# Kernel tuning notes

Measured on AMD Instinct MI355X. Metric: run time of the kernel, lower is better.

The kernel has to match this reference:

```python
import jax, jax.numpy as jnp
import numpy as np

N_NODES = 50000

def gcn_conv(x, edge_index, W, b):
    # PyG GCNConv default: add self-loops, symmetric norm D^-1/2 (A+I) D^-1/2, then XW + b
    n = x.shape[0]
    loop = jnp.arange(n, dtype=edge_index.dtype)
    src = jnp.concatenate([edge_index[0], loop])
    dst = jnp.concatenate([edge_index[1], loop])
    deg = jax.ops.segment_sum(jnp.ones_like(src, dtype=x.dtype), dst, num_segments=n)
    dinv = jnp.where(deg > 0, jax.lax.rsqrt(jnp.maximum(deg, 1e-12)), 0.0)
    norm = dinv[src] * dinv[dst]                      # [E+N]
    h = x @ W                                          # [N, d_out]
    msg = h[src] * norm[:, None]                       # gather + scale
    out = jax.ops.segment_sum(msg, dst, num_segments=n)  # scatter-add
    return out + b

def leaky(x):
    return jnp.where(x >= 0, x, 0.01 * x)

def setup_inputs() -> dict:
    key = jax.random.key(0)
    ks = jax.random.split(key, 10)
    x = jax.random.normal(ks[0], (N_NODES, 128), dtype=jnp.float32)
    edge_index = jax.random.randint(ks[1], (2, 800000), 0, N_NODES, dtype=jnp.int64)
    W1 = jax.random.normal(ks[2], (128, 512), dtype=jnp.float32) / np.sqrt(128)
    b1 = jnp.zeros((512,), dtype=jnp.float32)
    W3 = jax.random.normal(ks[3], (512, 128), dtype=jnp.float32) / np.sqrt(512)
    b3 = jnp.zeros((128,), dtype=jnp.float32)
    fc1_w = jax.random.normal(ks[4], (256, 128), dtype=jnp.float32) * np.sqrt(2.0 / 256)
    fc1_b = jnp.zeros((256,), dtype=jnp.float32)
    fc2_w = jax.random.normal(ks[5], (1, 256), dtype=jnp.float32) * np.sqrt(2.0 / 1)
    fc2_b = jnp.zeros((1,), dtype=jnp.float32)
    return {"x": x, "edge_index": edge_index, "W1": W1, "b1": b1, "W3": W3, "b3": b3,
            "fc1_w": fc1_w, "fc1_b": fc1_b, "fc2_w": fc2_w, "fc2_b": fc2_b}

def reference(x, edge_index, W1, b1, W3, b3, fc1_w, fc1_b, fc2_w, fc2_b):
    h = leaky(gcn_conv(x, edge_index, W1, b1))
    h = leaky(gcn_conv(h, edge_index, W3, b3))
    h = leaky(h @ fc1_w.T + fc1_b)
    h = h @ fc2_w.T + fc2_b
    return h.squeeze(-1)  # [N]
```

## Files before the change

### kernel.cpp

```cpp
#include <hip/hip_runtime.h>
#include <hip/hip_fp16.h>

typedef _Float16 f16x8 __attribute__((ext_vector_type(8)));
typedef __attribute__((ext_vector_type(4))) float f32x4;

static __device__ __forceinline__ float leaky(float v) { return v >= 0.f ? v : 0.01f * v; }

__global__ __launch_bounds__(256) void k_prep_all(
    const float* __restrict__ x, const float* __restrict__ W1, const float* __restrict__ W3,
    const float* __restrict__ fc1w, const float* __restrict__ fc2b,
    const int* __restrict__ dst, int* __restrict__ bucket_cnt,
    float* __restrict__ out, __half* __restrict__ x16, __half* __restrict__ t2,
    _Float16* __restrict__ W1f, _Float16* __restrict__ W3f, _Float16* __restrict__ F1f,
    int N, int E)
{
    __shared__ int bcnt[256];
    bcnt[threadIdx.x] = 0;
    __syncthreads();
    const int gsz = gridDim.x * 256;
    const int gtid = blockIdx.x * 256 + threadIdx.x;
    float ob = fc2b[0];
    for (int i = gtid; i < N; i += gsz) out[i] = ob;
    for (int i = gtid; i < 64; i += gsz) {
        ((__half2*)x16)[(size_t)N * 64 + i] = __floats2half2_rn(0.f, 0.f);
        ((__half2*)t2)[(size_t)N * 64 + i] = __floats2half2_rn(0.f, 0.f);
    }
    for (int i = gtid; i < 32 * 4 * 64 * 8; i += gsz) {
        int j = i & 7, l = (i >> 3) & 63, ks = (i >> 9) & 3, cb = i >> 11;
        int k = ks * 32 + (l >> 4) * 8 + j, n = cb * 16 + (l & 15);
        W1f[i] = (_Float16)W1[k * 512 + n];
    }
    for (int i = gtid; i < 8 * 16 * 64 * 8; i += gsz) {
        int j = i & 7, l = (i >> 3) & 63, ks = (i >> 9) & 15, cb = i >> 13;
        int k = ks * 32 + (l >> 4) * 8 + j, n = cb * 16 + (l & 15);
        W3f[i] = (_Float16)W3[k * 128 + n];
    }
    for (int i = gtid; i < 16 * 4 * 64 * 8; i += gsz) {
        int j = i & 7, l = (i >> 3) & 63, ks = (i >> 9) & 3, cb = i >> 11;
        int k = ks * 32 + (l >> 4) * 8 + j, n = cb * 16 + (l & 15);
        F1f[i] = (_Float16)fc1w[n * 128 + k];
    }
    for (int i = gtid; i < N * 64; i += gsz) {
        float2 f = ((const float2*)x)[i];
        ((__half2*)x16)[i] = __floats2half2_rn(f.x, f.y);
    }
    for (int e = gtid; e < E; e += gsz) atomicAdd(&bcnt[dst[e] >> 8], 1);
    __syncthreads();
    int c = bcnt[threadIdx.x];
    if (c > 0) atomicAdd(&bucket_cnt[threadIdx.x], c);
}

__global__ __launch_bounds__(256) void k_bscan(const int* __restrict__ bucket_cnt,
                                               int* __restrict__ bucket_base,
                                               int* __restrict__ bucket_cursor, int E) {
    __shared__ int s[256];
    int tx = threadIdx.x;
    int v = bucket_cnt[tx];
    s[tx] = v; __syncthreads();
    for (int off = 1; off < 256; off <<= 1) {
        int t = (tx >= off) ? s[tx - off] : 0;
        __syncthreads();
        s[tx] += t;
        __syncthreads();
    }
    int excl = s[tx] - v;
    bucket_base[tx] = excl;
    bucket_cursor[tx] = excl;
    if (tx == 0) bucket_base[256] = E;
}

__global__ __launch_bounds__(256) void k_bfill(const int* __restrict__ src, const int* __restrict__ dst,
                                               int* __restrict__ bucket_cursor,
                                               unsigned int* __restrict__ pairs, int E) {
    __shared__ int cnt[256];
    __shared__ int base[256];
    const int CH = 4096;
    int c0 = blockIdx.x * CH;
    int cend = c0 + CH < E ? c0 + CH : E;
    int tx = threadIdx.x;
    cnt[tx] = 0;
    __syncthreads();
    for (int i = c0 + tx; i < cend; i += 256) atomicAdd(&cnt[dst[i] >> 8], 1);
    __syncthreads();
    int myc = cnt[tx];
    int mybase = 0;
    if (myc > 0) mybase = atomicAdd(&bucket_cursor[tx], myc);
    __syncthreads();
    cnt[tx] = 0;
    base[tx] = mybase;
    __syncthreads();
    for (int i = c0 + tx; i < cend; i += 256) {
        int d = dst[i];
        int b = d >> 8;
        int pos = base[b] + atomicAdd(&cnt[b], 1);
        pairs[pos] = ((unsigned)(d & 255) << 24) | (unsigned)src[i];
    }
}

__global__ __launch_bounds__(256) void k_bsort(const unsigned int* __restrict__ pairs,
                                               const int* __restrict__ bucket_base,
                                               uint4* __restrict__ desc, float* __restrict__ dinv,
                                               int* __restrict__ csr, __half* __restrict__ x16,
                                               int N) {
    __shared__ int cnt[256], pre[256], cur[64];
    __shared__ float sdinv[256];
    __shared__ int stage[3584];
    const int B = blockIdx.x >> 2, q = blockIdx.x & 3;
    const int tx = threadIdx.x;
    const int pbase = bucket_base[B], pcnt = bucket_base[B + 1] - pbase;
    const int PB = pbase + B * 2048;
    cnt[tx] = 0;
    __syncthreads();
    for (int i = tx; i < pcnt; i += 256) atomicAdd(&cnt[pairs[pbase + i] >> 24], 1);
    __syncthreads();
    int deg = cnt[tx];
    int cnt8 = (deg + 8) & ~7;
    float dv = rsqrtf((float)deg + 1.0f);
    __syncthreads();
    cnt[tx] = cnt8;
    sdinv[tx] = dv;
    pre[tx] = cnt8;
    __syncthreads();
    for (int off = 1; off < 256; off <<= 1) {
        int t = (tx >= off) ? pre[tx - off] : 0;
        __syncthreads();
        pre[tx] += t;
        __syncthreads();
    }
    int excl = pre[tx] - cnt8;
    int node = B * 256 + tx;
    if (node < N) {
        desc[node] = make_uint4((unsigned)(PB + excl), (unsigned)(cnt8 >> 3),
                                __float_as_uint(dv), 0u);
        dinv[node] = dv;
    }
    __syncthreads();
    pre[tx] = excl;
    __syncthreads();
    const int d0 = q * 64;
    const int qstart8 = pre[d0];
    const int qcnt8 = pre[d0 + 63] + cnt[d0 + 63] - qstart8;
    if (tx < 64) cur[tx] = pre[d0 + tx] - qstart8 + 1;
    __syncthreads();
    if (qcnt8 <= 3584) {
        for (int i = tx; i < qcnt8; i += 256) stage[i] = N;
        __syncthreads();
        if (tx < 64) stage[pre[d0 + tx] - qstart8] = B * 256 + d0 + tx;
        for (int i = tx; i < pcnt; i += 256) {
            unsigned p = pairs[pbase + i];
            int dl = (int)(p >> 24) - d0;
            if ((unsigned)dl < 64u) {
                int pos = atomicAdd(&cur[dl], 1);
                stage[pos] = (int)(p & 0xFFFFFFu);
            }
        }
        __syncthreads();
        for (int i = tx; i < qcnt8; i += 256) csr[PB + qstart8 + i] = stage[i];
    } else {
        for (int i = tx; i < qcnt8; i += 256) csr[PB + qstart8 + i] = N;
        __syncthreads();
        if (tx < 64) csr[PB + pre[d0 + tx]] = B * 256 + d0 + tx;
        for (int i = tx; i < pcnt; i += 256) {
            unsigned p = pairs[pbase + i];
            int dl = (int)(p >> 24) - d0;
            if ((unsigned)dl < 64u) {
                int pos = atomicAdd(&cur[dl], 1);
                csr[PB + qstart8 + pos] = (int)(p & 0xFFFFFFu);
            }
        }
    }
    for (int i = tx; i < 64 * 64; i += 256) {
        int r = i >> 6, c = i & 63;
        int nd = B * 256 + q * 64 + r;
        if (nd < N) {
            float s = sdinv[q * 64 + r];
            float2 f = __half22float2(((__half2*)x16)[(size_t)nd * 64 + c]);
            ((__half2*)x16)[(size_t)nd * 64 + c] = __floats2half2_rn(f.x * s, f.y * s);
        }
    }
}

template <bool BIASACT>
__global__ __launch_bounds__(256) void k_gather(const __half* __restrict__ X,
                                                const uint4* __restrict__ desc,
                                                const int* __restrict__ csr,
                                                const float* __restrict__ bias,
                                                __half* __restrict__ outp, int N) {
    int wid = __builtin_amdgcn_readfirstlane((int)((blockIdx.x * 256 + threadIdx.x) >> 6));
    if (wid >= N) return;
    int lane = threadIdx.x & 63, c = lane * 2;
    uint4 d = desc[wid];
    int k0 = __builtin_amdgcn_readfirstlane((int)d.x);
    int nit = __builtin_amdgcn_readfirstlane((int)d.y);
    float di = __uint_as_float(d.z);
    float accx = 0.f, accy = 0.f;
    for (int it = 0; it < nit; ++it) {
        int kk = k0 + it * 8;
        int ss[8];
        #pragma unroll
        for (int i = 0; i < 8; ++i) ss[i] = csr[kk + i];
        #pragma unroll
        for (int i = 0; i < 8; ++i) {
            float2 f = __half22float2(*(const __half2*)(X + (size_t)ss[i] * 128 + c));
            accx += f.x;
            accy += f.y;
        }
    }
    accx *= di;
    accy *= di;
    if (BIASACT) {
        accx = leaky(accx + bias[c]);
        accy = leaky(accy + bias[c + 1]);
    }
    *(__half2*)(outp + (size_t)wid * 128 + c) = __floats2half2_rn(accx, accy);
}

__global__ __launch_bounds__(256, 2) void k_fused12(
    const __half* __restrict__ A1h, const _Float16* __restrict__ W1f,
    const _Float16* __restrict__ W3f, const float* __restrict__ b1,
    const float* __restrict__ dinv, __half* __restrict__ t2, int M)
{
    __shared__ __align__(16) _Float16 As[128 * 136];
    __shared__ __align__(16) _Float16 Hs[128 * 136];
    const int tid = threadIdx.x, lane = tid & 63, wid = tid >> 6;
    const int wr = wid >> 1, wc = wid & 1;
    const int m0 = blockIdx.x * 128;
    {
        const int r = tid >> 1, hf = tid & 1;
        int gr = m0 + r; if (gr >= M) gr = M - 1;
        const __half* Ar = A1h + (size_t)gr * 128;
        #pragma unroll
        for (int c = 0; c < 8; ++c) {
            int ch = hf * 8 + c;
            *(uint4*)(As + r * 136 + ch * 8) = *(const uint4*)(Ar + ch * 8);
        }
    }
    float bq[4][4];
    #pragma unroll
    for (int q = 0; q < 4; ++q)
        #pragma unroll
        for (int n = 0; n < 4; ++n)
            bq[q][n] = b1[q * 128 + wc * 64 + n * 16 + (lane & 15)];
    __syncthreads();

    const int arow = lane & 15, kch = (lane >> 4) * 8;
    f32x4 acc2[4][4] = {};
    #pragma unroll
    for (int q = 0; q < 4; ++q) {
        f32x4 acc1[4][4] = {};
        #pragma unroll
        for (int ks = 0; ks < 4; ++ks) {
            f16x8 af[4], bf[4];
            #pragma unroll
            for (int i = 0; i < 4; ++i)
                af[i] = *(const f16x8*)(As + (wr * 64 + i * 16 + arow) * 136 + ks * 32 + kch);
            #pragma unroll
            for (int n = 0; n < 4; ++n) {
                int cb = q * 8 + wc * 4 + n;
                bf[n] = *(const f16x8*)(W1f + ((size_t)(cb * 4 + ks) * 64 + lane) * 8);
            }
            #pragma unroll
            for (int i = 0; i < 4; ++i)
                #pragma unroll
                for (int n = 0; n < 4; ++n)
                    acc1[i][n] = __builtin_amdgcn_mfma_f32_16x16x32_f16(af[i], bf[n], acc1[i][n], 0, 0, 0);
        }
        __syncthreads();
        #pragma unroll
        for (int i = 0; i < 4; ++i)
            #pragma unroll
            for (int n = 0; n < 4; ++n)
                #pragma unroll
                for (int j = 0; j < 4; ++j) {
                    int row = wr * 64 + i * 16 + (lane >> 4) * 4 + j;
                    int col = wc * 64 + n * 16 + (lane & 15);
                    Hs[row * 136 + col] = (_Float16)leaky(acc1[i][n][j] + bq[q][n]);
                }
        __syncthreads();
        #pragma unroll
        for (int ks = 0; ks < 4; ++ks) {
            f16x8 af[4], bf[4];
            #pragma unroll
            for (int i = 0; i < 4; ++i)
                af[i] = *(const f16x8*)(Hs + (wr * 64 + i * 16 + arow) * 136 + ks * 32 + kch);
            #pragma unroll
            for (int n = 0; n < 4; ++n) {
                int cb = wc * 4 + n, ksg = q * 4 + ks;
                bf[n] = *(const f16x8*)(W3f + ((size_t)(cb * 16 + ksg) * 64 + lane) * 8);
            }
            #pragma unroll
            for (int i = 0; i < 4; ++i)
                #pragma unroll
                for (int n = 0; n < 4; ++n)
                    acc2[i][n] = __builtin_amdgcn_mfma_f32_16x16x32_f16(af[i], bf[n], acc2[i][n], 0, 0, 0);
        }
    }
    __syncthreads();
    #pragma unroll
    for (int i = 0; i < 4; ++i)
        #pragma unroll
        for (int j = 0; j < 4; ++j) {
            int row = wr * 64 + i * 16 + (lane >> 4) * 4 + j;
            int gr = m0 + row;
            float dv = dinv[gr < M ? gr : M - 1];
            #pragma unroll
            for (int n = 0; n < 4; ++n) {
                int col = wc * 64 + n * 16 + (lane & 15);
                Hs[row * 136 + col] = (_Float16)(acc2[i][n][j] * dv);
            }
        }
    __syncthreads();
    {
        const int r = tid >> 1, hf = tid & 1;
        int gr = m0 + r;
        if (gr < M) {
            #pragma unroll
            for (int c = 0; c < 8; ++c) {
                int ch = hf * 8 + c;
                *(uint4*)(t2 + (size_t)gr * 128 + ch * 8) = *(const uint4*)(Hs + r * 136 + ch * 8);
            }
        }
    }
}

__global__ __launch_bounds__(256, 2) void k_fgemm3(
    const __half* __restrict__ A3h, const _Float16* __restrict__ F1f,
    const float* __restrict__ fc1b, const float* __restrict__ fc2w,
    float* __restrict__ out, int M)
{
    __shared__ __align__(16) _Float16 As[128 * 136];
    const int tid = threadIdx.x, lane = tid & 63, wid = tid >> 6;
    const int wr = wid >> 1, wc = wid & 1;
    const int bx = blockIdx.x & 1, m0 = (blockIdx.x >> 1) * 128;
    const int nbase = bx * 128;
    {
        const int r = tid >> 1, hf = tid & 1;
        int gr = m0 + r; if (gr >= M) gr = M - 1;
        const __half* Ar = A3h + (size_t)gr * 128;
        #pragma unroll
        for (int c = 0; c < 8; ++c) {
            int ch = hf * 8 + c;
            *(uint4*)(As + r * 136 + ch * 8) = *(const uint4*)(Ar + ch * 8);
        }
    }
    __syncthreads();
    const int arow = lane & 15, kch = (lane >> 4) * 8;
    f32x4 acc[4][4] = {};
    #pragma unroll
    for (int ks = 0; ks < 4; ++ks) {
        f16x8 af[4], bf[4];
        #pragma unroll
        for (int i = 0; i < 4; ++i)
            af[i] = *(const f16x8*)(As + (wr * 64 + i * 16 + arow) * 136 + ks * 32 + kch);
        #pragma unroll
        for (int n = 0; n < 4; ++n) {
            int cb = bx * 8 + wc * 4 + n;
            bf[n] = *(const f16x8*)(F1f + ((size_t)(cb * 4 + ks) * 64 + lane) * 8);
        }
        #pragma unroll
        for (int i = 0; i < 4; ++i)
            #pragma unroll
            for (int n = 0; n < 4; ++n)
                acc[i][n] = __builtin_amdgcn_mfma_f32_16x16x32_f16(af[i], bf[n], acc[i][n], 0, 0, 0);
    }
    #pragma unroll
    for (int i = 0; i < 4; ++i)
        #pragma unroll
        for (int j = 0; j < 4; ++j) {
            int row = m0 + wr * 64 + i * 16 + (lane >> 4) * 4 + j;
            float s = 0.f;
            #pragma unroll
            for (int n = 0; n < 4; ++n) {
                int col = nbase + wc * 64 + n * 16 + (lane & 15);
                float v = leaky(acc[i][n][j] + fc1b[col]);
                s += v * fc2w[col];
            }
            s += __shfl_xor(s, 8);
            s += __shfl_xor(s, 4);
            s += __shfl_xor(s, 2);
            s += __shfl_xor(s, 1);
            if ((lane & 15) == 0 && row < M) atomicAdd(&out[row], s);
        }
}

extern "C" void kernel_launch(void* const* d_in, const int* in_sizes, int n_in,
                              void* d_out, int out_size, void* d_ws, size_t ws_size,
                              hipStream_t stream) {
    const float* x    = (const float*)d_in[0];
    const int*   ei   = (const int*)d_in[1];
    const float* W1   = (const float*)d_in[2];
    const float* b1   = (const float*)d_in[3];
    const float* W3   = (const float*)d_in[4];
    const float* b3   = (const float*)d_in[5];
    const float* fc1w = (const float*)d_in[6];
    const float* fc1b = (const float*)d_in[7];
    const float* fc2w = (const float*)d_in[8];
    const float* fc2b = (const float*)d_in[9];
    float* out = (float*)d_out;

    int N = in_sizes[0] / 128;
    int E = in_sizes[1] / 2;
    const int* src = ei;
    const int* dst = ei + E;

    const int NB = (N + 255) >> 8;
    char* ws = (char*)d_ws;
    size_t off = 0;
    auto alloc = [&](size_t bytes) { void* p = ws + off; off += (bytes + 255) & ~255ull; return p; };
    int*   bucket_cnt    = (int*)alloc(257 * 4);
    int*   bucket_base   = (int*)alloc(257 * 4);
    int*   bucket_cursor = (int*)alloc(257 * 4);
    uint4* desc   = (uint4*)alloc((size_t)N * 16);
    unsigned int* pairs = (unsigned int*)alloc((size_t)E * 4);
    int*   csr    = (int*)alloc(((size_t)E + (size_t)NB * 2048) * 4);
    float* dinv   = (float*)alloc((size_t)N * 4);
    __half* x16   = (__half*)alloc((size_t)(N + 1) * 128 * 2);
    __half* A1h   = (__half*)alloc((size_t)N * 128 * 2);
    __half* t2    = (__half*)alloc((size_t)(N + 1) * 128 * 2);
    __half* A3h   = (__half*)alloc((size_t)N * 128 * 2);
    _Float16* W1f = (_Float16*)alloc((size_t)32 * 4 * 64 * 8 * 2);
    _Float16* W3f = (_Float16*)alloc((size_t)8 * 16 * 64 * 8 * 2);
    _Float16* F1f = (_Float16*)alloc((size_t)16 * 4 * 64 * 8 * 2);
    (void)ws_size; (void)n_in; (void)out_size;

    const int MB128 = (N + 127) / 128;
    dim3 blk(256);

    hipMemsetAsync(bucket_cnt, 0, 257 * 4, stream);

    k_prep_all<<<1024, blk, 0, stream>>>(x, W1, W3, fc1w, fc2b, dst, bucket_cnt,
                                         out, x16, t2, W1f, W3f, F1f, N, E);
    k_bscan<<<1, blk, 0, stream>>>(bucket_cnt, bucket_base, bucket_cursor, E);
    k_bfill<<<(E + 4095) / 4096, blk, 0, stream>>>(src, dst, bucket_cursor, pairs, E);
    k_bsort<<<NB * 4, blk, 0, stream>>>(pairs, bucket_base, desc, dinv, csr, x16, N);
    k_gather<false><<<(N * 64 + 255) / 256, blk, 0, stream>>>(x16, desc, csr, nullptr, A1h, N);
    k_fused12<<<MB128, blk, 0, stream>>>(A1h, W1f, W3f, b1, dinv, t2, N);
    k_gather<true><<<(N * 64 + 255) / 256, blk, 0, stream>>>(t2, desc, csr, b3, A3h, N);
    k_fgemm3<<<MB128 * 2, blk, 0, stream>>>(A3h, F1f, fc1b, fc2w, out, N);
}
```

Before: 246.8 us.

## Pad CSR rows to 16 and shrink fused GEMM tile to 64 rows

Each node's CSR neighbor list is now padded to a multiple of 16 instead of 8, so the gather loop issues 16 independent row loads per iteration for more memory-level parallelism. This costs more padding reads of the zero row and a larger CSR buffer. Separately, the fused two-layer GEMM now uses 64-row tiles with each wave owning a 32-column slice, halving its shared memory and raising the occupancy hint to 4 blocks per SIMD. The smaller tile gives more blocks but less reuse of the weight loads per block.

```diff
diff --git a/kernel.cpp b/kernel.cpp
--- a/kernel.cpp
+++ b/kernel.cpp
@@ -108,18 +108,18 @@
     const int B = blockIdx.x >> 2, q = blockIdx.x & 3;
     const int tx = threadIdx.x;
     const int pbase = bucket_base[B], pcnt = bucket_base[B + 1] - pbase;
-    const int PB = pbase + B * 2048;
+    const int PB = pbase + B * 8192;
     cnt[tx] = 0;
     __syncthreads();
     for (int i = tx; i < pcnt; i += 256) atomicAdd(&cnt[pairs[pbase + i] >> 24], 1);
     __syncthreads();
     int deg = cnt[tx];
-    int cnt8 = (deg + 8) & ~7;
+    int cnt16 = (deg + 16) & ~15;
     float dv = rsqrtf((float)deg + 1.0f);
     __syncthreads();
-    cnt[tx] = cnt8;
+    cnt[tx] = cnt16;
     sdinv[tx] = dv;
-    pre[tx] = cnt8;
+    pre[tx] = cnt16;
     __syncthreads();
     for (int off = 1; off < 256; off <<= 1) {
         int t = (tx >= off) ? pre[tx - off] : 0;
@@ -127,10 +127,10 @@
         pre[tx] += t;
         __syncthreads();
     }
-    int excl = pre[tx] - cnt8;
+    int excl = pre[tx] - cnt16;
     int node = B * 256 + tx;
     if (node < N) {
-        desc[node] = make_uint4((unsigned)(PB + excl), (unsigned)(cnt8 >> 3),
+        desc[node] = make_uint4((unsigned)(PB + excl), (unsigned)(cnt16 >> 4),
                                 __float_as_uint(dv), 0u);
         dinv[node] = dv;
     }
@@ -138,14 +138,14 @@
     pre[tx] = excl;
     __syncthreads();
     const int d0 = q * 64;
-    const int qstart8 = pre[d0];
-    const int qcnt8 = pre[d0 + 63] + cnt[d0 + 63] - qstart8;
-    if (tx < 64) cur[tx] = pre[d0 + tx] - qstart8 + 1;
-    __syncthreads();
-    if (qcnt8 <= 3584) {
-        for (int i = tx; i < qcnt8; i += 256) stage[i] = N;
-        __syncthreads();
-        if (tx < 64) stage[pre[d0 + tx] - qstart8] = B * 256 + d0 + tx;
+    const int qstart = pre[d0];
+    const int qcnt = pre[d0 + 63] + cnt[d0 + 63] - qstart;
+    if (tx < 64) cur[tx] = pre[d0 + tx] - qstart + 1;
+    __syncthreads();
+    if (qcnt <= 3584) {
+        for (int i = tx; i < qcnt; i += 256) stage[i] = N;
+        __syncthreads();
+        if (tx < 64) stage[pre[d0 + tx] - qstart] = B * 256 + d0 + tx;
         for (int i = tx; i < pcnt; i += 256) {
             unsigned p = pairs[pbase + i];
             int dl = (int)(p >> 24) - d0;
@@ -155,9 +155,9 @@
             }
         }
         __syncthreads();
-        for (int i = tx; i < qcnt8; i += 256) csr[PB + qstart8 + i] = stage[i];
+        for (int i = tx; i < qcnt; i += 256) csr[PB + qstart + i] = stage[i];
     } else {
-        for (int i = tx; i < qcnt8; i += 256) csr[PB + qstart8 + i] = N;
+        for (int i = tx; i < qcnt; i += 256) csr[PB + qstart + i] = N;
         __syncthreads();
         if (tx < 64) csr[PB + pre[d0 + tx]] = B * 256 + d0 + tx;
         for (int i = tx; i < pcnt; i += 256) {
@@ -165,7 +165,7 @@
             int dl = (int)(p >> 24) - d0;
             if ((unsigned)dl < 64u) {
                 int pos = atomicAdd(&cur[dl], 1);
-                csr[PB + qstart8 + pos] = (int)(p & 0xFFFFFFu);
+                csr[PB + qstart + pos] = (int)(p & 0xFFFFFFu);
             }
         }
     }
@@ -195,12 +195,12 @@
     float di = __uint_as_float(d.z);
     float accx = 0.f, accy = 0.f;
     for (int it = 0; it < nit; ++it) {
-        int kk = k0 + it * 8;
-        int ss[8];
-        #pragma unroll
-        for (int i = 0; i < 8; ++i) ss[i] = csr[kk + i];
-        #pragma unroll
-        for (int i = 0; i < 8; ++i) {
+        int kk = k0 + it * 16;
+        int ss[16];
+        #pragma unroll
+        for (int i = 0; i < 16; ++i) ss[i] = csr[kk + i];
+        #pragma unroll
+        for (int i = 0; i < 16; ++i) {
             float2 f = __half22float2(*(const __half2*)(X + (size_t)ss[i] * 128 + c));
             accx += f.x;
             accy += f.y;
@@ -215,83 +215,82 @@
     *(__half2*)(outp + (size_t)wid * 128 + c) = __floats2half2_rn(accx, accy);
 }
 
-__global__ __launch_bounds__(256, 2) void k_fused12(
+__global__ __launch_bounds__(256, 4) void k_fused12(
     const __half* __restrict__ A1h, const _Float16* __restrict__ W1f,
     const _Float16* __restrict__ W3f, const float* __restrict__ b1,
     const float* __restrict__ dinv, __half* __restrict__ t2, int M)
 {
-    __shared__ __align__(16) _Float16 As[128 * 136];
-    __shared__ __align__(16) _Float16 Hs[128 * 136];
+    __shared__ __align__(16) _Float16 As[64 * 136];
+    __shared__ __align__(16) _Float16 Hs[64 * 136];
     const int tid = threadIdx.x, lane = tid & 63, wid = tid >> 6;
-    const int wr = wid >> 1, wc = wid & 1;
-    const int m0 = blockIdx.x * 128;
+    const int m0 = blockIdx.x * 64;
     {
-        const int r = tid >> 1, hf = tid & 1;
+        const int r = tid >> 2, cq = tid & 3;
         int gr = m0 + r; if (gr >= M) gr = M - 1;
         const __half* Ar = A1h + (size_t)gr * 128;
         #pragma unroll
-        for (int c = 0; c < 8; ++c) {
-            int ch = hf * 8 + c;
+        for (int cc = 0; cc < 4; ++cc) {
+            int ch = cq * 4 + cc;
             *(uint4*)(As + r * 136 + ch * 8) = *(const uint4*)(Ar + ch * 8);
         }
     }
-    float bq[4][4];
+    float bq[4][2];
     #pragma unroll
     for (int q = 0; q < 4; ++q)
         #pragma unroll
-        for (int n = 0; n < 4; ++n)
-            bq[q][n] = b1[q * 128 + wc * 64 + n * 16 + (lane & 15)];
+        for (int n = 0; n < 2; ++n)
+            bq[q][n] = b1[q * 128 + wid * 32 + n * 16 + (lane & 15)];
     __syncthreads();
 
     const int arow = lane & 15, kch = (lane >> 4) * 8;
-    f32x4 acc2[4][4] = {};
+    f32x4 acc2[4][2] = {};
     #pragma unroll
     for (int q = 0; q < 4; ++q) {
-        f32x4 acc1[4][4] = {};
+        f32x4 acc1[4][2] = {};
         #pragma unroll
         for (int ks = 0; ks < 4; ++ks) {
-            f16x8 af[4], bf[4];
+            f16x8 af[4], bf[2];
             #pragma unroll
             for (int i = 0; i < 4; ++i)
-                af[i] = *(const f16x8*)(As + (wr * 64 + i * 16 + arow) * 136 + ks * 32 + kch);
-            #pragma unroll
-            for (int n = 0; n < 4; ++n) {
-                int cb = q * 8 + wc * 4 + n;
+                af[i] = *(const f16x8*)(As + (i * 16 + arow) * 136 + ks * 32 + kch);
+            #pragma unroll
+            for (int n = 0; n < 2; ++n) {
+                int cb = q * 8 + wid * 2 + n;
                 bf[n] = *(const f16x8*)(W1f + ((size_t)(cb * 4 + ks) * 64 + lane) * 8);
             }
             #pragma unroll
             for (int i = 0; i < 4; ++i)
                 #pragma unroll
-                for (int n = 0; n < 4; ++n)
+                for (int n = 0; n < 2; ++n)
                     acc1[i][n] = __builtin_amdgcn_mfma_f32_16x16x32_f16(af[i], bf[n], acc1[i][n], 0, 0, 0);
         }
         __syncthreads();
         #pragma unroll
         for (int i = 0; i < 4; ++i)
             #pragma unroll
-            for (int n = 0; n < 4; ++n)
+            for (int n = 0; n < 2; ++n)
                 #pragma unroll
                 for (int j = 0; j < 4; ++j) {
-                    int row = wr * 64 + i * 16 + (lane >> 4) * 4 + j;
-                    int col = wc * 64 + n * 16 + (lane & 15);
+                    int row = i * 16 + (lane >> 4) * 4 + j;
+                    int col = wid * 32 + n * 16 + (lane & 15);
                     Hs[row * 136 + col] = (_Float16)leaky(acc1[i][n][j] + bq[q][n]);
                 }
         __syncthreads();
         #pragma unroll
         for (int ks = 0; ks < 4; ++ks) {
-            f16x8 af[4], bf[4];
+            f16x8 af[4], bf[2];
             #pragma unroll
             for (int i = 0; i < 4; ++i)
-                af[i] = *(const f16x8*)(Hs + (wr * 64 + i * 16 + arow) * 136 + ks * 32 + kch);
-            #pragma unroll
-            for (int n = 0; n < 4; ++n) {
-                int cb = wc * 4 + n, ksg = q * 4 + ks;
+                af[i] = *(const f16x8*)(Hs + (i * 16 + arow) * 136 + ks * 32 + kch);
+            #pragma unroll
+            for (int n = 0; n < 2; ++n) {
+                int cb = wid * 2 + n, ksg = q * 4 + ks;
                 bf[n] = *(const f16x8*)(W3f + ((size_t)(cb * 16 + ksg) * 64 + lane) * 8);
             }
             #pragma unroll
             for (int i = 0; i < 4; ++i)
                 #pragma unroll
-                for (int n = 0; n < 4; ++n)
+                for (int n = 0; n < 2; ++n)
                     acc2[i][n] = __builtin_amdgcn_mfma_f32_16x16x32_f16(af[i], bf[n], acc2[i][n], 0, 0, 0);
         }
     }
@@ -300,23 +299,23 @@
     for (int i = 0; i < 4; ++i)
         #pragma unroll
         for (int j = 0; j < 4; ++j) {
-            int row = wr * 64 + i * 16 + (lane >> 4) * 4 + j;
+            int row = i * 16 + (lane >> 4) * 4 + j;
             int gr = m0 + row;
             float dv = dinv[gr < M ? gr : M - 1];
             #pragma unroll
-            for (int n = 0; n < 4; ++n) {
-                int col = wc * 64 + n * 16 + (lane & 15);
+            for (int n = 0; n < 2; ++n) {
+                int col = wid * 32 + n * 16 + (lane & 15);
                 Hs[row * 136 + col] = (_Float16)(acc2[i][n][j] * dv);
             }
         }
     __syncthreads();
     {
-        const int r = tid >> 1, hf = tid & 1;
+        const int r = tid >> 2, cq = tid & 3;
         int gr = m0 + r;
         if (gr < M) {
             #pragma unroll
-            for (int c = 0; c < 8; ++c) {
-                int ch = hf * 8 + c;
+            for (int cc = 0; cc < 4; ++cc) {
+                int ch = cq * 4 + cc;
                 *(uint4*)(t2 + (size_t)gr * 128 + ch * 8) = *(const uint4*)(Hs + r * 136 + ch * 8);
             }
         }
@@ -412,7 +411,7 @@
     int*   bucket_cursor = (int*)alloc(257 * 4);
     uint4* desc   = (uint4*)alloc((size_t)N * 16);
     unsigned int* pairs = (unsigned int*)alloc((size_t)E * 4);
-    int*   csr    = (int*)alloc(((size_t)E + (size_t)NB * 2048) * 4);
+    int*   csr    = (int*)alloc(((size_t)E + (size_t)NB * 8192) * 4);
     float* dinv   = (float*)alloc((size_t)N * 4);
     __half* x16   = (__half*)alloc((size_t)(N + 1) * 128 * 2);
     __half* A1h   = (__half*)alloc((size_t)N * 128 * 2);
@@ -424,6 +423,7 @@
     (void)ws_size; (void)n_in; (void)out_size;
 
     const int MB128 = (N + 127) / 128;
+    const int MB64  = (N + 63) / 64;
     dim3 blk(256);
 
     hipMemsetAsync(bucket_cnt, 0, 257 * 4, stream);
@@ -434,7 +434,7 @@
     k_bfill<<<(E + 4095) / 4096, blk, 0, stream>>>(src, dst, bucket_cursor, pairs, E);
     k_bsort<<<NB * 4, blk, 0, stream>>>(pairs, bucket_base, desc, dinv, csr, x16, N);
     k_gather<false><<<(N * 64 + 255) / 256, blk, 0, stream>>>(x16, desc, csr, nullptr, A1h, N);
-    k_fused12<<<MB128, blk, 0, stream>>>(A1h, W1f, W3f, b1, dinv, t2, N);
+    k_fused12<<<MB64, blk, 0, stream>>>(A1h, W1f, W3f, b1, dinv, t2, N);
     k_gather<true><<<(N * 64 + 255) / 256, blk, 0, stream>>>(t2, desc, csr, b3, A3h, N);
     k_fgemm3<<<MB128 * 2, blk, 0, stream>>>(A3h, F1f, fc1b, fc2w, out, N);
 }
```

Result: no change. 245.2 us (-0.6%).
